# Kernel tuning notes

Hardware: AMD Instinct MI355X
Metric: run time of the kernel (lower is better)

The kernel has to match this reference:

```python
import jax, jax.numpy as jnp
import numpy as np

N_U, N_P, E = 200000, 50000, 500000
D_U, D_P, H, OUT = 100, 50, 128, 1
BN_EPS = 1e-5


def _lin(k, dout, din):
    s = 1.0 / np.sqrt(din)
    kw, kb = jax.random.split(k)
    W = jax.random.uniform(kw, (dout, din), jnp.float32, -s, s)
    b = jax.random.uniform(kb, (dout,), jnp.float32, -s, s)
    return W, b


def setup_inputs() -> dict:
    key = jax.random.key(0)
    ks = jax.random.split(key, 12)
    x_u = jax.random.normal(ks[0], (N_U, D_U), jnp.float32)
    x_p = jax.random.normal(ks[1], (N_P, D_P), jnp.float32)
    src = jax.random.randint(ks[2], (E,), 0, N_U, jnp.int64) if jax.config.jax_enable_x64 else jax.random.randint(ks[2], (E,), 0, N_U)
    dst = jax.random.randint(ks[3], (E,), N_U, N_U + N_P)
    edge_index = jnp.stack([src, dst]).astype(jnp.int32)
    W_u, b_u = _lin(ks[4], H, D_U)
    W_p, b_p = _lin(ks[5], H, D_P)
    W1l, b1l = _lin(ks[6], H, H)   # SAGEConv lin_l (aggregated neighbors, carries bias)
    W1r, _ = _lin(ks[7], H, H)     # SAGEConv lin_r (root, no bias)
    W2l, b2l = _lin(ks[8], H, H)
    W2r, _ = _lin(ks[9], H, H)
    W_out, b_out = _lin(ks[10], OUT, H)
    return dict(x_u=x_u, x_p=x_p, edge_index=edge_index,
                W_u=W_u, b_u=b_u, W_p=W_p, b_p=b_p,
                W1l=W1l, b1l=b1l, W1r=W1r,
                g1=jnp.ones((H,), jnp.float32), be1=jnp.zeros((H,), jnp.float32),
                W2l=W2l, b2l=b2l, W2r=W2r,
                g2=jnp.ones((H,), jnp.float32), be2=jnp.zeros((H,), jnp.float32),
                W_out=W_out, b_out=b_out)


def reference(x_u, x_p, edge_index, W_u, b_u, W_p, b_p,
              W1l, b1l, W1r, g1, be1, W2l, b2l, W2r, g2, be2,
              W_out, b_out):
    N = x_u.shape[0] + x_p.shape[0]
    # input projections + relu, then concat users/products -> [N, H]
    x = jnp.concatenate([jax.nn.relu(x_u @ W_u.T + b_u),
                         jax.nn.relu(x_p @ W_p.T + b_p)], axis=0)
    # to_undirected: add reversed edges (bipartite => no duplicates)
    src = jnp.concatenate([edge_index[0], edge_index[1]])
    dst = jnp.concatenate([edge_index[1], edge_index[0]])
    deg = jnp.maximum(jax.ops.segment_sum(jnp.ones_like(dst, jnp.float32), dst, num_segments=N), 1.0)

    def sage(h, Wl, bl, Wr):
        # mean aggregation of neighbor features, scatter by dst
        mean = jax.ops.segment_sum(h[src], dst, num_segments=N) / deg[:, None]
        return mean @ Wl.T + bl + h @ Wr.T

    def bn(h, g, b):
        m = h.mean(0)
        v = h.var(0)  # biased variance, as used for normalization in torch BN
        return (h - m) * jax.lax.rsqrt(v + BN_EPS) * g + b

    h1 = jax.nn.relu(bn(sage(x, W1l, b1l, W1r), g1, be1))   # dropout = identity (eval)
    h2 = jax.nn.relu(bn(sage(h1, W2l, b2l, W2r), g2, be2)) + x
    return h2[: x_u.shape[0]] @ W_out.T + b_out
```

## Files before the change

kernel.cpp:

```cpp
#include <hip/hip_runtime.h>
#include <hip/hip_bf16.h>
#include <cstdint>
#include <cstddef>

#define NT   250000
#define NUU  200000
#define NPP  50000
#define EG   500000
#define E2   1000000
#define HD   128
#define NBLK_SCAN 977

#define CNT2_OFF   0ull
#define SPART2_OFF 1000000ull
#define SS2_OFF    1065536ull
#define RPTR2_OFF  1067584ull
#define BSUM2_OFF  2067588ull
#define BMAT2_OFF  2071504ull
#define COL2_OFF   2251728ull
#define X2_OFF     6251728ull
#define R1B_OFF    70251728ull
#define C2_OFF     134251728ull
#define WS_SPLIT   198251728ull

typedef __hip_bfloat16 bf16;
typedef __attribute__((ext_vector_type(8))) short short8v;
typedef __attribute__((ext_vector_type(4))) float f32x4;

__device__ inline float b2f(short s) { return __builtin_bit_cast(float, ((unsigned)(unsigned short)s) << 16); }
__device__ inline unsigned short f2bf(float f) { return __builtin_bit_cast(unsigned short, __float2bfloat16(f)); }

__global__ __launch_bounds__(256) void k_zero(int* __restrict__ p, int n) {
    for (int i = blockIdx.x * 256 + threadIdx.x; i < n; i += gridDim.x * 256) p[i] = 0;
}

__global__ __launch_bounds__(256) void k_count(const int* __restrict__ ei, int* __restrict__ cnt) {
    for (int e = blockIdx.x * 256 + threadIdx.x; e < E2; e += gridDim.x * 256) {
        int d = (e < EG) ? ei[e + EG] : ei[e - EG];
        atomicAdd(&cnt[d], 1);
    }
}

__global__ __launch_bounds__(256) void k_scan1(const int* __restrict__ cnt, int* __restrict__ bsum) {
    __shared__ int lds[256];
    int i = blockIdx.x * 256 + threadIdx.x;
    int v = (i < NT) ? cnt[i] : 0;
    lds[threadIdx.x] = v; __syncthreads();
    for (int s = 128; s > 0; s >>= 1) {
        if (threadIdx.x < s) lds[threadIdx.x] += lds[threadIdx.x + s];
        __syncthreads();
    }
    if (threadIdx.x == 0) bsum[blockIdx.x] = lds[0];
}

__global__ __launch_bounds__(1024) void k_scan2(int* __restrict__ bsum) {
    __shared__ int lds[1024];
    int i = threadIdx.x;
    int v = (i < NBLK_SCAN) ? bsum[i] : 0;
    lds[i] = v; __syncthreads();
    for (int off = 1; off < 1024; off <<= 1) {
        int t = (i >= off) ? lds[i - off] : 0;
        __syncthreads();
        lds[i] += t;
        __syncthreads();
    }
    if (i < NBLK_SCAN) bsum[i] = lds[i] - v;
}

__global__ __launch_bounds__(256) void k_scan3(const int* __restrict__ cnt, const int* __restrict__ bsum,
                                               int* __restrict__ rp) {
    __shared__ int lds[256];
    int i = blockIdx.x * 256 + threadIdx.x;
    int v = (i < NT) ? cnt[i] : 0;
    lds[threadIdx.x] = v; __syncthreads();
    for (int off = 1; off < 256; off <<= 1) {
        int t = (threadIdx.x >= off) ? lds[threadIdx.x - off] : 0;
        __syncthreads();
        lds[threadIdx.x] += t;
        __syncthreads();
    }
    if (i < NT) rp[i] = bsum[blockIdx.x] + lds[threadIdx.x] - v;
    if (i == 0 && blockIdx.x == 0) rp[NT] = E2;
}

__global__ __launch_bounds__(256) void k_fill(const int* __restrict__ ei, const int* __restrict__ rp,
                                              int* __restrict__ fill, int* __restrict__ col) {
    for (int e = blockIdx.x * 256 + threadIdx.x; e < E2; e += gridDim.x * 256) {
        int s = ei[e];
        int d = (e < EG) ? ei[e + EG] : ei[e - EG];
        int slot = rp[d] + atomicAdd(&fill[d], 1);
        col[slot] = s;
    }
}

__global__ __launch_bounds__(256) void k_wcvt(const float* __restrict__ W1l, const float* __restrict__ W1r,
                                              const float* __restrict__ W2l, const float* __restrict__ W2r,
                                              const float* __restrict__ Wu, const float* __restrict__ Wp,
                                              bf16* __restrict__ B) {
    int i = blockIdx.x * 256 + threadIdx.x;
    if (i < 65536) {
        int layer = i >> 15, rem = i & 32767, o = rem >> 8, k = rem & 255;
        const float* W = layer ? ((k < 128) ? W2l : W2r) : ((k < 128) ? W1l : W1r);
        B[i] = __float2bfloat16(W[o * 128 + (k & 127)]);
    } else if (i < 81920) {
        int rem = i - 65536, o = rem >> 7, k = rem & 127;
        B[i] = __float2bfloat16((k < 100) ? Wu[o * 100 + k] : 0.f);
    } else if (i < 90112) {
        int rem = i - 81920, o = rem >> 6, k = rem & 63;
        B[i] = __float2bfloat16((k < 50) ? Wp[o * 50 + k] : 0.f);
    }
}

template<int DIN, int KPAD>
__global__ __launch_bounds__(256) void k_projm(const float* __restrict__ in, const bf16* __restrict__ Bp,
                                               const float* __restrict__ bias, bf16* __restrict__ outp,
                                               int nrows, int rowbase) {
    __shared__ __align__(16) char As[128 * KPAD * 2];
    const int tid = threadIdx.x;
    const int tb = blockIdx.x * 128;
    constexpr int RSTRIDE = KPAD * 2;
    constexpr int PADE = KPAD - DIN;
    constexpr int PH = PADE / 2;
    constexpr int PPAD = 128 * PH;
    constexpr int PMAIN = 128 * DIN / 2;

    for (int q = tid; q < PPAD; q += 256) {
        int row = q / PH;
        int k = DIN + (q - row * PH) * 2;
        *(unsigned*)(As + row * RSTRIDE + ((((k >> 3) << 4) ^ ((row & 7) << 4)) + (k & 7) * 2)) = 0u;
    }
    for (int q = tid; q < PMAIN; q += 256) {
        int f = q * 2;
        int row = f / DIN, k = f - row * DIN;
        int rg = tb + row; if (rg > nrows - 1) rg = nrows - 1;
        float2 v = *(const float2*)(in + (size_t)rg * DIN + k);
        unsigned u = (unsigned)f2bf(v.x) | ((unsigned)f2bf(v.y) << 16);
        *(unsigned*)(As + row * RSTRIDE + ((((k >> 3) << 4) ^ ((row & 7) << 4)) + (k & 7) * 2)) = u;
    }
    __syncthreads();

    const int lane = tid & 63, wid = tid >> 6;
    const int wr = wid >> 1, wc = wid & 1;
    const int r15 = lane & 15, l4 = lane >> 4;
    constexpr int NKS = KPAD / 32;
    f32x4 acc[4][4] = {};
#pragma unroll
    for (int ks = 0; ks < NKS; ks++) {
        short8v a[4], b[4];
#pragma unroll
        for (int m = 0; m < 4; m++) {
            int rl = wr * 64 + m * 16 + r15;
            a[m] = *(const short8v*)(As + rl * RSTRIDE + ((ks * 64 + l4 * 16) ^ ((rl & 7) << 4)));
        }
#pragma unroll
        for (int n = 0; n < 4; n++) {
            int c = wc * 64 + n * 16 + r15;
            b[n] = *(const short8v*)(Bp + (size_t)c * KPAD + ks * 32 + l4 * 8);
        }
#pragma unroll
        for (int m = 0; m < 4; m++)
#pragma unroll
            for (int n = 0; n < 4; n++)
                acc[m][n] = __builtin_amdgcn_mfma_f32_16x16x32_bf16(a[m], b[n], acc[m][n], 0, 0, 0);
    }
    float bcol[4];
#pragma unroll
    for (int n = 0; n < 4; n++) bcol[n] = bias[wc * 64 + n * 16 + r15];
#pragma unroll
    for (int m = 0; m < 4; m++)
#pragma unroll
        for (int n = 0; n < 4; n++)
#pragma unroll
            for (int g = 0; g < 4; g++) {
                int row = tb + wr * 64 + m * 16 + l4 * 4 + g;
                if (row < nrows) {
                    float v = fmaxf(acc[m][n][g] + bcol[n], 0.f);
                    outp[(size_t)(rowbase + row) * HD + wc * 64 + n * 16 + r15] = __float2bfloat16(v);
                }
            }
}

template<bool NORM>
__global__ __launch_bounds__(256) void k_spmm(const bf16* __restrict__ hin, const float* __restrict__ ssv,
                                              const int* __restrict__ rp, const int* __restrict__ col,
                                              bf16* __restrict__ M) {
    const int tid = threadIdx.x;
    const int gid = tid >> 3, l8 = tid & 7;
    const int fo = l8 * 8;
    float sva[8], tva[8], svb[8], tvb[8];
    if (NORM) {
#pragma unroll
        for (int j = 0; j < 8; j++) {
            sva[j] = ssv[fo + j];      tva[j] = ssv[HD + fo + j];
            svb[j] = ssv[64 + fo + j]; tvb[j] = ssv[HD + 64 + fo + j];
        }
    }
    for (int n = blockIdx.x * 32 + gid; n < NT; n += gridDim.x * 32) {
        int s0 = rp[n], s1 = rp[n + 1];
        float a[8] = {}, b[8] = {};
        for (int p = s0; p < s1; p += 4) {
            int i1 = min(p + 1, s1 - 1), i2 = min(p + 2, s1 - 1), i3 = min(p + 3, s1 - 1);
            int c0 = col[p], c1 = col[i1], c2 = col[i2], c3 = col[i3];
            const bf16* r0p = hin + (size_t)c0 * HD + fo;
            const bf16* r1p = hin + (size_t)c1 * HD + fo;
            const bf16* r2p = hin + (size_t)c2 * HD + fo;
            const bf16* r3p = hin + (size_t)c3 * HD + fo;
            short8v uA0 = *(const short8v*)r0p, uB0 = *(const short8v*)(r0p + 64);
            short8v uA1 = *(const short8v*)r1p, uB1 = *(const short8v*)(r1p + 64);
            short8v uA2 = *(const short8v*)r2p, uB2 = *(const short8v*)(r2p + 64);
            short8v uA3 = *(const short8v*)r3p, uB3 = *(const short8v*)(r3p + 64);
            float m1 = (p + 1 < s1) ? 1.f : 0.f;
            float m2 = (p + 2 < s1) ? 1.f : 0.f;
            float m3 = (p + 3 < s1) ? 1.f : 0.f;
#pragma unroll
            for (int j = 0; j < 8; j++) {
                float vA0 = b2f(uA0[j]), vA1 = b2f(uA1[j]), vA2 = b2f(uA2[j]), vA3 = b2f(uA3[j]);
                float vB0 = b2f(uB0[j]), vB1 = b2f(uB1[j]), vB2 = b2f(uB2[j]), vB3 = b2f(uB3[j]);
                if (NORM) {
                    vA0 = fmaxf(fmaf(vA0, sva[j], tva[j]), 0.f);
                    vA1 = fmaxf(fmaf(vA1, sva[j], tva[j]), 0.f);
                    vA2 = fmaxf(fmaf(vA2, sva[j], tva[j]), 0.f);
                    vA3 = fmaxf(fmaf(vA3, sva[j], tva[j]), 0.f);
                    vB0 = fmaxf(fmaf(vB0, svb[j], tvb[j]), 0.f);
                    vB1 = fmaxf(fmaf(vB1, svb[j], tvb[j]), 0.f);
                    vB2 = fmaxf(fmaf(vB2, svb[j], tvb[j]), 0.f);
                    vB3 = fmaxf(fmaf(vB3, svb[j], tvb[j]), 0.f);
                }
                a[j] += vA0 + m1 * vA1 + m2 * vA2 + m3 * vA3;
                b[j] += vB0 + m1 * vB1 + m2 * vB2 + m3 * vB3;
            }
        }
        float inv = 1.f / (float)max(s1 - s0, 1);
        short8v wa, wb;
#pragma unroll
        for (int j = 0; j < 8; j++) { wa[j] = (short)f2bf(a[j] * inv); wb[j] = (short)f2bf(b[j] * inv); }
        *(short8v*)(M + (size_t)n * HD + fo) = wa;
        *(short8v*)(M + (size_t)n * HD + 64 + fo) = wb;
    }
}

template<bool NORM>
__global__ __launch_bounds__(256) void k_dense(const bf16* __restrict__ Min, const bf16* __restrict__ hin,
                                               const float* __restrict__ ssv,
                                               const bf16* __restrict__ Bmat, const float* __restrict__ blv,
                                               bf16* __restrict__ outp, float* __restrict__ spart,
                                               int store_n) {
    __shared__ __align__(16) char At[32768];
    const int tid = threadIdx.x;
    const int seg = tid & 15, r0 = tid >> 4;
    const int fo = seg * 8;
    const int tb = blockIdx.x * 128;

    float sv[8], tv[8];
    if (NORM) {
#pragma unroll
        for (int j = 0; j < 8; j++) { sv[j] = ssv[fo + j]; tv[j] = ssv[HD + fo + j]; }
    }

    const int lane = tid & 63, wid = tid >> 6;
    const int wr = wid >> 1, wc = wid & 1;
    const int r15 = lane & 15, l4 = lane >> 4;
    f32x4 acc[4][4] = {};

#pragma unroll
    for (int it = 0; it < 8; it++) {
        int row = r0 + it * 16;
        int r = tb + row; if (r > NT - 1) r = NT - 1;
        short8v v = *(const short8v*)(Min + (size_t)r * HD + fo);
        *(short8v*)(At + row * 256 + ((seg * 16) ^ ((row & 7) << 4))) = v;
    }
    __syncthreads();
#pragma unroll
    for (int ks = 0; ks < 4; ks++) {
        short8v a[4], b[4];
#pragma unroll
        for (int m = 0; m < 4; m++) {
            int rl = wr * 64 + m * 16 + r15;
            a[m] = *(const short8v*)(At + rl * 256 + ((ks * 64 + l4 * 16) ^ ((rl & 7) << 4)));
        }
#pragma unroll
        for (int n = 0; n < 4; n++) {
            int c = wc * 64 + n * 16 + r15;
            b[n] = *(const short8v*)(Bmat + (size_t)c * 256 + ks * 32 + l4 * 8);
        }
#pragma unroll
        for (int m = 0; m < 4; m++)
#pragma unroll
            for (int n = 0; n < 4; n++)
                acc[m][n] = __builtin_amdgcn_mfma_f32_16x16x32_bf16(a[m], b[n], acc[m][n], 0, 0, 0);
    }
    __syncthreads();

#pragma unroll
    for (int it = 0; it < 8; it++) {
        int row = r0 + it * 16;
        int r = tb + row; if (r > NT - 1) r = NT - 1;
        short8v v = *(const short8v*)(hin + (size_t)r * HD + fo);
        if (NORM) {
#pragma unroll
            for (int j = 0; j < 8; j++) {
                float f = b2f(v[j]);
                v[j] = (short)f2bf(fmaxf(fmaf(f, sv[j], tv[j]), 0.f));
            }
        }
        *(short8v*)(At + row * 256 + ((seg * 16) ^ ((row & 7) << 4))) = v;
    }
    __syncthreads();
#pragma unroll
    for (int ks = 0; ks < 4; ks++) {
        short8v a[4], b[4];
#pragma unroll
        for (int m = 0; m < 4; m++) {
            int rl = wr * 64 + m * 16 + r15;
            a[m] = *(const short8v*)(At + rl * 256 + ((ks * 64 + l4 * 16) ^ ((rl & 7) << 4)));
        }
#pragma unroll
        for (int n = 0; n < 4; n++) {
            int c = wc * 64 + n * 16 + r15;
            b[n] = *(const short8v*)(Bmat + (size_t)c * 256 + (ks + 4) * 32 + l4 * 8);
        }
#pragma unroll
        for (int m = 0; m < 4; m++)
#pragma unroll
            for (int n = 0; n < 4; n++)
                acc[m][n] = __builtin_amdgcn_mfma_f32_16x16x32_bf16(a[m], b[n], acc[m][n], 0, 0, 0);
    }

    float bcol[4];
#pragma unroll
    for (int n = 0; n < 4; n++) bcol[n] = blv[wc * 64 + n * 16 + r15];
    float ls[4] = {0.f, 0.f, 0.f, 0.f}, lq[4] = {0.f, 0.f, 0.f, 0.f};
#pragma unroll
    for (int m = 0; m < 4; m++)
#pragma unroll
        for (int n = 0; n < 4; n++)
#pragma unroll
            for (int gg = 0; gg < 4; gg++) {
                int row = tb + wr * 64 + m * 16 + l4 * 4 + gg;
                float v = acc[m][n][gg] + bcol[n];
                if (row < NT) { ls[n] += v; lq[n] += v * v; }
                if (row < store_n)
                    outp[(size_t)row * HD + wc * 64 + n * 16 + r15] = __float2bfloat16(v);
            }
    int part = (blockIdx.x & 31) * 256;
#pragma unroll
    for (int n = 0; n < 4; n++) {
        float s = ls[n], q2 = lq[n];
        s  += __shfl_xor(s, 16);  s  += __shfl_xor(s, 32);
        q2 += __shfl_xor(q2, 16); q2 += __shfl_xor(q2, 32);
        if (l4 == 0) {
            atomicAdd(&spart[part + wc * 64 + n * 16 + r15], s);
            atomicAdd(&spart[part + 128 + wc * 64 + n * 16 + r15], q2);
        }
    }
}

__global__ void k_fin(const float* __restrict__ sp, const float* __restrict__ g,
                      const float* __restrict__ be, float* __restrict__ ssout) {
    int j = threadIdx.x;
    float m = 0.f, q = 0.f;
    for (int i = 0; i < 32; i++) { m += sp[i * 256 + j]; q += sp[i * 256 + 128 + j]; }
    m *= (1.f / (float)NT);
    q = q * (1.f / (float)NT) - m * m;
    float s = g[j] * rsqrtf(q + 1e-5f);
    ssout[j] = s;
    ssout[HD + j] = be[j] - m * s;
}

__global__ __launch_bounds__(256) void k_out(const bf16* __restrict__ r2, const float* __restrict__ ss,
                                             const bf16* __restrict__ x, const float* __restrict__ wout,
                                             const float* __restrict__ bout, float* __restrict__ outp) {
    int lane = threadIdx.x & 63;
    int wv = (blockIdx.x * blockDim.x + threadIdx.x) >> 6;
    int nwv = (gridDim.x * blockDim.x) >> 6;
    int g16 = lane >> 4, l16 = lane & 15;
    int fo = l16 * 8;
    float s8[8], t8[8], w8[8];
#pragma unroll
    for (int j = 0; j < 8; j++) {
        s8[j] = ss[fo + j]; t8[j] = ss[HD + fo + j]; w8[j] = wout[fo + j];
    }
    float bo = bout[0];
    for (int r0 = wv * 4; r0 < NUU; r0 += nwv * 4) {
        int row = r0 + g16;
        short8v a  = *(const short8v*)(r2 + (size_t)row * HD + fo);
        short8v xx = *(const short8v*)(x  + (size_t)row * HD + fo);
        float acc = 0.f;
#pragma unroll
        for (int j = 0; j < 8; j++) {
            float h = fmaxf(fmaf(b2f(a[j]), s8[j], t8[j]), 0.f) + b2f(xx[j]);
            acc += h * w8[j];
        }
        acc += __shfl_xor(acc, 1);
        acc += __shfl_xor(acc, 2);
        acc += __shfl_xor(acc, 4);
        acc += __shfl_xor(acc, 8);
        if (l16 == 0) outp[row] = acc + bo;
    }
}

extern "C" void kernel_launch(void* const* d_in, const int* in_sizes, int n_in,
                              void* d_out, int out_size, void* d_ws, size_t ws_size,
                              hipStream_t stream) {
    const float* x_u = (const float*)d_in[0];
    const float* x_p = (const float*)d_in[1];
    const int*   ei  = (const int*)d_in[2];
    const float* W_u = (const float*)d_in[3];
    const float* b_u = (const float*)d_in[4];
    const float* W_p = (const float*)d_in[5];
    const float* b_p = (const float*)d_in[6];
    const float* W1l = (const float*)d_in[7];
    const float* b1l = (const float*)d_in[8];
    const float* W1r = (const float*)d_in[9];
    const float* g1  = (const float*)d_in[10];
    const float* be1 = (const float*)d_in[11];
    const float* W2l = (const float*)d_in[12];
    const float* b2l = (const float*)d_in[13];
    const float* W2r = (const float*)d_in[14];
    const float* g2  = (const float*)d_in[15];
    const float* be2 = (const float*)d_in[16];
    const float* Wout = (const float*)d_in[17];
    const float* bout = (const float*)d_in[18];
    float* out = (float*)d_out;
    char* ws = (char*)d_ws;

    if (ws_size < WS_SPLIT) {
        k_zero<<<512, 256, 0, stream>>>((int*)d_out, out_size);
        return;
    }

    int*  cnt    = (int*)(ws + CNT2_OFF);
    float* spart = (float*)(ws + SPART2_OFF);
    float* ssbuf = (float*)(ws + SS2_OFF);
    int*  rp     = (int*)(ws + RPTR2_OFF);
    int*  bsum   = (int*)(ws + BSUM2_OFF);
    bf16* Bmat   = (bf16*)(ws + BMAT2_OFF);
    int*  col    = (int*)(ws + COL2_OFF);
    bf16* X      = (bf16*)(ws + X2_OFF);
    bf16* R1     = (bf16*)(ws + R1B_OFF);
    bf16* MC     = (bf16*)(ws + C2_OFF);

    k_zero<<<1043, 256, 0, stream>>>(cnt, 266896);
    k_wcvt<<<352, 256, 0, stream>>>(W1l, W1r, W2l, W2r, W_u, W_p, Bmat);

    k_count<<<1024, 256, 0, stream>>>(ei, cnt);
    k_scan1<<<NBLK_SCAN, 256, 0, stream>>>(cnt, bsum);
    k_scan2<<<1, 1024, 0, stream>>>(bsum);
    k_scan3<<<NBLK_SCAN, 256, 0, stream>>>(cnt, bsum, rp);
    k_zero<<<977, 256, 0, stream>>>(cnt, NT);
    k_fill<<<1024, 256, 0, stream>>>(ei, rp, cnt, col);

    k_projm<100, 128><<<1563, 256, 0, stream>>>(x_u, Bmat + 65536, b_u, X, NUU, 0);
    k_projm<50, 64><<<391, 256, 0, stream>>>(x_p, Bmat + 81920, b_p, X, NPP, NUU);

    k_spmm<false><<<2048, 256, 0, stream>>>(X, nullptr, rp, col, MC);
    k_dense<false><<<1954, 256, 0, stream>>>(MC, X, nullptr, Bmat, b1l, R1, spart, NT);
    k_fin<<<1, 128, 0, stream>>>(spart, g1, be1, ssbuf);

    k_spmm<true><<<2048, 256, 0, stream>>>(R1, ssbuf, rp, col, MC);
    k_dense<true><<<1954, 256, 0, stream>>>(MC, R1, ssbuf, Bmat + 32768, b2l, MC, spart + 8192, NUU);
    k_fin<<<1, 128, 0, stream>>>(spart + 8192, g2, be2, ssbuf + 256);

    k_out<<<1024, 256, 0, stream>>>(MC, ssbuf + 256, X, Wout, bout, out);
}
```

Baseline: 472.6 us.

## Fuse SpMM mean aggregation with dense SAGE GEMM into one layer kernel

Merges the neighbor-mean SpMM and the dense MFMA GEMM into a single kernel per layer. Each block aggregates its 128 nodes directly into shared memory, so the intermediate mean matrix never round-trips through global memory, and one launch per layer is removed. Root-feature rows are prefetched into registers before the first GEMM. In exchange the gather phase now runs with the GEMM's tiling, at 4 nodes per 8-lane group and 1954 blocks, which may hurt load balance on skewed degrees. The larger register footprint (vh buffer) may also lower occupancy.

```diff
diff --git a/kernel.cpp b/kernel.cpp
--- a/kernel.cpp
+++ b/kernel.cpp
@@ -20,7 +20,7 @@
 #define COL2_OFF   2251728ull
 #define X2_OFF     6251728ull
 #define R1B_OFF    70251728ull
-#define C2_OFF     134251728ull
+#define R2B_OFF    134251728ull
 #define WS_SPLIT   198251728ull
 
 typedef __hip_bfloat16 bf16;
@@ -181,10 +181,15 @@
 }
 
 template<bool NORM>
-__global__ __launch_bounds__(256) void k_spmm(const bf16* __restrict__ hin, const float* __restrict__ ssv,
-                                              const int* __restrict__ rp, const int* __restrict__ col,
-                                              bf16* __restrict__ M) {
+__global__ __launch_bounds__(256) void k_layer(const bf16* __restrict__ hin, const float* __restrict__ ssv,
+                                               const int* __restrict__ rp, const int* __restrict__ col,
+                                               const bf16* __restrict__ Bmat, const float* __restrict__ blv,
+                                               bf16* __restrict__ outp, float* __restrict__ spart,
+                                               int store_n) {
+    __shared__ __align__(16) char At[32768];
     const int tid = threadIdx.x;
+    const int tb = blockIdx.x * 128;
+
     const int gid = tid >> 3, l8 = tid & 7;
     const int fo = l8 * 8;
     float sva[8], tva[8], svb[8], tvb[8];
@@ -195,8 +200,11 @@
             svb[j] = ssv[64 + fo + j]; tvb[j] = ssv[HD + 64 + fo + j];
         }
     }
-    for (int n = blockIdx.x * 32 + gid; n < NT; n += gridDim.x * 32) {
-        int s0 = rp[n], s1 = rp[n + 1];
+    for (int q = 0; q < 4; q++) {
+        int nl = q * 32 + gid;
+        int node = tb + nl;
+        int s0 = 0, s1 = 0;
+        if (node < NT) { s0 = rp[node]; s1 = rp[node + 1]; }
         float a[8] = {}, b[8] = {};
         for (int p = s0; p < s1; p += 4) {
             int i1 = min(p + 1, s1 - 1), i2 = min(p + 2, s1 - 1), i3 = min(p + 3, s1 - 1);
@@ -234,42 +242,25 @@
         short8v wa, wb;
 #pragma unroll
         for (int j = 0; j < 8; j++) { wa[j] = (short)f2bf(a[j] * inv); wb[j] = (short)f2bf(b[j] * inv); }
-        *(short8v*)(M + (size_t)n * HD + fo) = wa;
-        *(short8v*)(M + (size_t)n * HD + 64 + fo) = wb;
-    }
-}
-
-template<bool NORM>
-__global__ __launch_bounds__(256) void k_dense(const bf16* __restrict__ Min, const bf16* __restrict__ hin,
-                                               const float* __restrict__ ssv,
-                                               const bf16* __restrict__ Bmat, const float* __restrict__ blv,
-                                               bf16* __restrict__ outp, float* __restrict__ spart,
-                                               int store_n) {
-    __shared__ __align__(16) char At[32768];
-    const int tid = threadIdx.x;
+        *(short8v*)(At + nl * 256 + ((l8 * 16) ^ ((nl & 7) << 4))) = wa;
+        *(short8v*)(At + nl * 256 + (((8 + l8) * 16) ^ ((nl & 7) << 4))) = wb;
+    }
+
     const int seg = tid & 15, r0 = tid >> 4;
-    const int fo = seg * 8;
-    const int tb = blockIdx.x * 128;
-
-    float sv[8], tv[8];
-    if (NORM) {
-#pragma unroll
-        for (int j = 0; j < 8; j++) { sv[j] = ssv[fo + j]; tv[j] = ssv[HD + fo + j]; }
-    }
+    const int sfo = seg * 8;
+    short8v vh[8];
+#pragma unroll
+    for (int it = 0; it < 8; it++) {
+        int row = r0 + it * 16;
+        int r = tb + row; if (r > NT - 1) r = NT - 1;
+        vh[it] = *(const short8v*)(hin + (size_t)r * HD + sfo);
+    }
+    __syncthreads();
 
     const int lane = tid & 63, wid = tid >> 6;
     const int wr = wid >> 1, wc = wid & 1;
     const int r15 = lane & 15, l4 = lane >> 4;
     f32x4 acc[4][4] = {};
-
-#pragma unroll
-    for (int it = 0; it < 8; it++) {
-        int row = r0 + it * 16;
-        int r = tb + row; if (r > NT - 1) r = NT - 1;
-        short8v v = *(const short8v*)(Min + (size_t)r * HD + fo);
-        *(short8v*)(At + row * 256 + ((seg * 16) ^ ((row & 7) << 4))) = v;
-    }
-    __syncthreads();
 #pragma unroll
     for (int ks = 0; ks < 4; ks++) {
         short8v a[4], b[4];
@@ -291,21 +282,26 @@
     }
     __syncthreads();
 
+    if (NORM) {
+        float sv2[8], tv2[8];
+#pragma unroll
+        for (int j = 0; j < 8; j++) { sv2[j] = ssv[sfo + j]; tv2[j] = ssv[HD + sfo + j]; }
+#pragma unroll
+        for (int it = 0; it < 8; it++) {
+#pragma unroll
+            for (int j = 0; j < 8; j++) {
+                float f = b2f(vh[it][j]);
+                vh[it][j] = (short)f2bf(fmaxf(fmaf(f, sv2[j], tv2[j]), 0.f));
+            }
+        }
+    }
 #pragma unroll
     for (int it = 0; it < 8; it++) {
         int row = r0 + it * 16;
-        int r = tb + row; if (r > NT - 1) r = NT - 1;
-        short8v v = *(const short8v*)(hin + (size_t)r * HD + fo);
-        if (NORM) {
-#pragma unroll
-            for (int j = 0; j < 8; j++) {
-                float f = b2f(v[j]);
-                v[j] = (short)f2bf(fmaxf(fmaf(f, sv[j], tv[j]), 0.f));
-            }
-        }
-        *(short8v*)(At + row * 256 + ((seg * 16) ^ ((row & 7) << 4))) = v;
+        *(short8v*)(At + row * 256 + ((seg * 16) ^ ((row & 7) << 4))) = vh[it];
     }
     __syncthreads();
+
 #pragma unroll
     for (int ks = 0; ks < 4; ks++) {
         short8v a[4], b[4];
@@ -438,7 +434,7 @@
     int*  col    = (int*)(ws + COL2_OFF);
     bf16* X      = (bf16*)(ws + X2_OFF);
     bf16* R1     = (bf16*)(ws + R1B_OFF);
-    bf16* MC     = (bf16*)(ws + C2_OFF);
+    bf16* R2     = (bf16*)(ws + R2B_OFF);
 
     k_zero<<<1043, 256, 0, stream>>>(cnt, 266896);
     k_wcvt<<<352, 256, 0, stream>>>(W1l, W1r, W2l, W2r, W_u, W_p, Bmat);
@@ -453,13 +449,11 @@
     k_projm<100, 128><<<1563, 256, 0, stream>>>(x_u, Bmat + 65536, b_u, X, NUU, 0);
     k_projm<50, 64><<<391, 256, 0, stream>>>(x_p, Bmat + 81920, b_p, X, NPP, NUU);
 
-    k_spmm<false><<<2048, 256, 0, stream>>>(X, nullptr, rp, col, MC);
-    k_dense<false><<<1954, 256, 0, stream>>>(MC, X, nullptr, Bmat, b1l, R1, spart, NT);
+    k_layer<false><<<1954, 256, 0, stream>>>(X, nullptr, rp, col, Bmat, b1l, R1, spart, NT);
     k_fin<<<1, 128, 0, stream>>>(spart, g1, be1, ssbuf);
 
-    k_spmm<true><<<2048, 256, 0, stream>>>(R1, ssbuf, rp, col, MC);
-    k_dense<true><<<1954, 256, 0, stream>>>(MC, R1, ssbuf, Bmat + 32768, b2l, MC, spart + 8192, NUU);
+    k_layer<true><<<1954, 256, 0, stream>>>(R1, ssbuf, rp, col, Bmat + 32768, b2l, R2, spart + 8192, NUU);
     k_fin<<<1, 128, 0, stream>>>(spart + 8192, g2, be2, ssbuf + 256);
 
-    k_out<<<1024, 256, 0, stream>>>(MC, ssbuf + 256, X, Wout, bout, out);
-}
+    k_out<<<1024, 256, 0, stream>>>(R2, ssbuf + 256, X, Wout, bout, out);
+}
```

After: 436.0 us. -7.8%, faster.
